# Kernel tuning notes

Measured on AMD Instinct MI355X. Metric: run time of the kernel, lower is better.

## Reference

```python
import jax, jax.numpy as jnp
import numpy as np

NUM_HEADS = 16
THETA = 10000.0


def _rotate_half(x):
    # interleaved pairs: (..., d) -> pairs (x1, x2) -> (-x2, x1) interleaved back
    x = x.reshape(x.shape[:-1] + (-1, 2))
    x1, x2 = x[..., 0], x[..., 1]
    return jnp.stack((-x2, x1), axis=-1).reshape(x.shape[:-2] + (-1,))


def _rope(x):
    # x: [B, H, S, d_k]
    d_k = x.shape[-1]
    seq_len = x.shape[-2]
    inv_freq = 1.0 / (THETA ** (jnp.arange(0, d_k, 2, dtype=jnp.float32) / d_k))  # [d_k/2]
    pos = jnp.arange(seq_len, dtype=jnp.float32)  # [S]
    theta = pos[:, None] * inv_freq[None, :]  # [S, d_k/2]
    cos = jnp.repeat(jnp.cos(theta), 2, axis=-1)  # [S, d_k]
    sin = jnp.repeat(jnp.sin(theta), 2, axis=-1)
    return x * cos + _rotate_half(x) * sin


def setup_inputs() -> dict:
    key = jax.random.key(0)
    kx, kq, kk, kv, ko = jax.random.split(key, 5)
    B, S, D = 2, 2048, 1024
    std = 1.0 / (2.0 * (2 * D) ** 0.5)
    return {
        "x": jax.random.normal(kx, (B, S, D), dtype=jnp.float32),
        "Wq": jax.random.normal(kq, (D, D), dtype=jnp.float32) * std,
        "Wk": jax.random.normal(kk, (D, D), dtype=jnp.float32) * std,
        "Wv": jax.random.normal(kv, (D, D), dtype=jnp.float32) * std,
        "Wo": jax.random.normal(ko, (D, D), dtype=jnp.float32) * std,
    }


def reference(x, Wq, Wk, Wv, Wo):
    B, S, D = x.shape
    H = NUM_HEADS
    d_k = D // H

    def split_heads(t):  # [B,S,D] -> [B,H,S,d_k]
        return t.reshape(B, S, H, d_k).transpose(0, 2, 1, 3)

    Q = split_heads(x @ Wq)
    K = split_heads(x @ Wk)
    V = split_heads(x @ Wv)

    Q = _rope(Q)
    K = _rope(K)

    scores = jnp.einsum("bhqd,bhkd->bhqk", Q, K) / jnp.sqrt(jnp.float32(d_k))
    causal = jnp.tril(jnp.ones((S, S), dtype=bool))  # [S,S]
    scores = jnp.where(causal[None, None], scores, -jnp.inf)
    attn = jax.nn.softmax(scores, axis=-1)
    out = jnp.einsum("bhqk,bhkd->bhqd", attn, V)  # [B,H,S,d_k]
    out = out.transpose(0, 2, 1, 3).reshape(B, S, D)
    return out @ Wo
```

## Files before the change

kernel.cpp:

```cpp
#include <hip/hip_runtime.h>
#include <cmath>


constexpr int Bz = 2, Sq = 2048, Dm = 1024, Hh = 16, DK = 64;
constexpr int Mrows = Bz * Sq;

typedef __attribute__((ext_vector_type(4))) float f32x4;
typedef __attribute__((ext_vector_type(2))) __bf16 bf16x2;
typedef __attribute__((ext_vector_type(4))) __bf16 bf16x4;
typedef __attribute__((ext_vector_type(8))) __bf16 bf16x8;
typedef __attribute__((ext_vector_type(8))) short short8v;

__device__ __forceinline__ f32x4 mfma16(bf16x8 a, bf16x8 b, f32x4 c) {
  return __builtin_amdgcn_mfma_f32_16x16x32_bf16(a, b, c, 0, 0, 0);
}
__device__ __forceinline__ short bfb(float x) {
  return __builtin_bit_cast(short, (__bf16)x);
}
__device__ __forceinline__ float fexp2(float x) {
#if __has_builtin(__builtin_amdgcn_exp2f)
  return __builtin_amdgcn_exp2f(x);
#else
  float r;
  asm("v_exp_f32 %0, %1" : "=v"(r) : "v"(x));
  return r;
#endif
}
__device__ __forceinline__ void gload16(const void* g, void* l) {
  __builtin_amdgcn_global_load_lds(
      (__attribute__((address_space(1))) void*)g,
      (__attribute__((address_space(3))) void*)l, 16, 0, 0);
}

__global__ __launch_bounds__(256) void prep_kernel(
    const float* __restrict__ x, const float* __restrict__ Wq,
    const float* __restrict__ Wk, const float* __restrict__ Wv,
    const float* __restrict__ Wo, __bf16* __restrict__ xb,
    __bf16* __restrict__ Wt, float2* __restrict__ tbl) {
  __shared__ float tile[32][33];
  const int bid = blockIdx.x, tid = threadIdx.x;
  if (bid < 2048) {
    int t = bid * 256 + tid;
    const float4* p = (const float4*)x + (size_t)t * 2;
    float4 a = p[0], b = p[1];
    bf16x8 o = {(__bf16)a.x, (__bf16)a.y, (__bf16)a.z, (__bf16)a.w,
                (__bf16)b.x, (__bf16)b.y, (__bf16)b.z, (__bf16)b.w};
    *(bf16x8*)(xb + (size_t)t * 8) = o;
  } else if (bid < 6144) {
    int wid = bid - 2048;
    int z = wid >> 10, rem = wid & 1023;
    const float* W = (z == 0) ? Wq : (z == 1) ? Wk : (z == 2) ? Wv : Wo;
    __bf16* out = Wt + (size_t)z * Dm * Dm;
    int r0 = (rem >> 5) * 32, c0 = (rem & 31) * 32;
    int r = tid >> 3, c4 = (tid & 7) * 4;
    float4 v = *(const float4*)&W[(size_t)(r0 + r) * Dm + c0 + c4];
    tile[r][c4] = v.x; tile[r][c4 + 1] = v.y;
    tile[r][c4 + 2] = v.z; tile[r][c4 + 3] = v.w;
    __syncthreads();
    int nl = tid >> 3, k4 = (tid & 7) * 4;
    bf16x4 o = {(__bf16)tile[k4][nl], (__bf16)tile[k4 + 1][nl],
                (__bf16)tile[k4 + 2][nl], (__bf16)tile[k4 + 3][nl]};
    *(bf16x4*)&out[(size_t)(c0 + nl) * Dm + r0 + k4] = o;
  } else {
    int t = (bid - 6144) * 256 + tid;
    int s = t >> 5, j = t & 31;
    float inv = exp2f(-13.287712379549449f * (1.0f / 32.0f) * (float)j);
    float sn, cs;
    sincosf((float)s * inv, &sn, &cs);
    tbl[t] = make_float2(cs, sn);
  }
}

__device__ __forceinline__ void gemm_core(const __bf16* __restrict__ A,
                                          const __bf16* __restrict__ Bt,
                                          char* smem, f32x4 (&acc)[4][4],
                                          int m0, int n0, int tid) {
  short* As = (short*)smem;
  short* Bs = (short*)(smem + 16384);
  const int lane = tid & 63, w = tid >> 6;
  const int qi = lane & 15, c = lane >> 4;
  const int wr = w >> 1, wc = w & 1;
  const int srow = lane >> 2, scol = (lane & 3) * 8;
  const __bf16* gA = A + (size_t)(m0 + w * 16 + srow) * Dm + scol;
  const __bf16* gB = Bt + (size_t)(n0 + w * 16 + srow) * Dm + scol;
  short* lA = As + w * 512;
  short* lB = Bs + w * 512;

  auto stage = [&](int cb, int k0) {
    gload16(gA + k0, lA + cb * 4096);
    gload16(gA + (size_t)64 * Dm + k0, lA + cb * 4096 + 2048);
    gload16(gB + k0, lB + cb * 4096);
    gload16(gB + (size_t)64 * Dm + k0, lB + cb * 4096 + 2048);
  };

#pragma unroll
  for (int i = 0; i < 4; ++i)
#pragma unroll
    for (int j = 0; j < 4; ++j) acc[i][j] = (f32x4){0.f, 0.f, 0.f, 0.f};

  stage(0, 0);
  __syncthreads();
  int cur = 0;
  for (int k0 = 0; k0 < Dm; k0 += 32) {
    if (k0 + 32 < Dm) stage(cur ^ 1, k0 + 32);
    bf16x8 af[4], bfv[4];
#pragma unroll
    for (int i = 0; i < 4; ++i) {
      af[i]  = *(bf16x8*)(As + cur * 4096 + (wr * 64 + i * 16 + qi) * 32 + c * 8);
      bfv[i] = *(bf16x8*)(Bs + cur * 4096 + (wc * 64 + i * 16 + qi) * 32 + c * 8);
    }
#pragma unroll
    for (int i = 0; i < 4; ++i)
#pragma unroll
      for (int j = 0; j < 4; ++j) acc[i][j] = mfma16(af[i], bfv[j], acc[i][j]);
    __syncthreads();
    cur ^= 1;
  }
}

__global__ __launch_bounds__(256) void gemm_qkv(
    const __bf16* __restrict__ xb, const __bf16* __restrict__ Wt,
    const float2* __restrict__ tbl, __bf16* __restrict__ Qb,
    __bf16* __restrict__ Kb, __bf16* __restrict__ Vt) {
  __shared__ __align__(16) char smem[34816];
  const int tid = threadIdx.x;
  const int bid = blockIdx.x;
  const int xcd = bid & 7, r8 = bid >> 3;
  const int mb = (xcd << 2) | (r8 & 3);
  const int zn = r8 >> 2;
  const int z = zn >> 3, nb = zn & 7;
  const int m0 = mb * 128, n0 = nb * 128;

  f32x4 acc[4][4];
  gemm_core(xb, Wt + (size_t)z * Dm * Dm, smem, acc, m0, n0, tid);

  const int lane = tid & 63, w = tid >> 6;
  const int qi = lane & 15, c = lane >> 4;
  const int wr = w >> 1, wc = w & 1;

  if (z == 2) {
    __syncthreads();
    short* T = (short*)smem;
#pragma unroll
    for (int i = 0; i < 4; ++i)
#pragma unroll
      for (int j = 0; j < 4; ++j) {
        int nl = wc * 64 + j * 16 + qi;
        int mbr = wr * 64 + i * 16 + c * 4;
        bf16x4 pk = {(__bf16)acc[i][j][0], (__bf16)acc[i][j][1],
                     (__bf16)acc[i][j][2], (__bf16)acc[i][j][3]};
        *(bf16x4*)(T + nl * 136 + mbr) = pk;
      }
    __syncthreads();
    short* C = (short*)Vt;
    int b = m0 >> 11, sb = m0 & (Sq - 1);
#pragma unroll
    for (int it = 0; it < 8; ++it) {
      int f = tid + it * 256;
      int nl = f >> 4, mc = f & 15;
      short8v v = *(short8v*)(T + nl * 136 + mc * 8);
      int ng = n0 + nl;
      int d = ng & (DK - 1), h = (ng >> 6) & (Hh - 1);
      *(short8v*)(C + ((size_t)(b * Hh + h) * DK + d) * Sq + sb + mc * 8) = v;
    }
  } else {
    __syncthreads();
    short* T = (short*)smem;
#pragma unroll
    for (int i = 0; i < 4; ++i)
#pragma unroll
      for (int j = 0; j < 4; ++j) {
        int nl = wc * 64 + j * 16 + qi;
        int mbr = wr * 64 + i * 16 + c * 4;
#pragma unroll
        for (int rr = 0; rr < 4; ++rr)
          T[(mbr + rr) * 136 + nl] = bfb(acc[i][j][rr]);
      }
    __syncthreads();
    const float sc = (z == 0) ? 0.18033688011112042f : 1.0f;
    short* C = (short*)((z == 0) ? Qb : Kb);
    const int b = m0 >> 11;
#pragma unroll
    for (int it = 0; it < 8; ++it) {
      int f = tid + it * 256;
      int ml = f >> 4, c16 = f & 15;
      bf16x8 v = *(bf16x8*)(T + ml * 136 + c16 * 8);
      int s = (m0 + ml) & (Sq - 1);
      int n = n0 + c16 * 8;
      int d0 = n & (DK - 1), h = (n >> 6) & (Hh - 1);
      int jj = d0 >> 1;
      float4 t01 = *(const float4*)&tbl[s * 32 + jj];
      float4 t23 = *(const float4*)&tbl[s * 32 + jj + 2];
      bf16x8 o;
      float x0 = (float)v[0], y0 = (float)v[1];
      o[0] = (__bf16)((x0 * t01.x - y0 * t01.y) * sc);
      o[1] = (__bf16)((y0 * t01.x + x0 * t01.y) * sc);
      float x1 = (float)v[2], y1 = (float)v[3];
      o[2] = (__bf16)((x1 * t01.z - y1 * t01.w) * sc);
      o[3] = (__bf16)((y1 * t01.z + x1 * t01.w) * sc);
      float x2 = (float)v[4], y2 = (float)v[5];
      o[4] = (__bf16)((x2 * t23.x - y2 * t23.y) * sc);
      o[5] = (__bf16)((y2 * t23.x + x2 * t23.y) * sc);
      float x3 = (float)v[6], y3 = (float)v[7];
      o[6] = (__bf16)((x3 * t23.z - y3 * t23.w) * sc);
      o[7] = (__bf16)((y3 * t23.z + x3 * t23.w) * sc);
      *(bf16x8*)(C + ((size_t)(b * Hh + h) * Sq + s) * DK + d0) = o;
    }
  }
}

__global__ __launch_bounds__(256) void gemm_o(
    const __bf16* __restrict__ AOb, const __bf16* __restrict__ Wto,
    float* __restrict__ C) {
  __shared__ __align__(16) char smem[34816];
  const int tid = threadIdx.x;
  const int bid = blockIdx.x;
  const int xcd = bid & 7, r8 = bid >> 3;
  const int mb = (xcd << 2) | (r8 & 3);
  const int nb = r8 >> 2;
  const int m0 = mb * 128, n0 = nb * 128;

  f32x4 acc[4][4];
  gemm_core(AOb, Wto, smem, acc, m0, n0, tid);

  const int lane = tid & 63, w = tid >> 6;
  const int qi = lane & 15, c = lane >> 4;
  const int wr = w >> 1, wc = w & 1;
  float* T32 = (float*)smem;

#pragma unroll
  for (int pass = 0; pass < 2; ++pass) {
    __syncthreads();
#pragma unroll
    for (int i2 = 0; i2 < 2; ++i2) {
      int i = pass * 2 + i2;
#pragma unroll
      for (int j = 0; j < 4; ++j) {
        int nl = wc * 64 + j * 16 + qi;
        int cm = wr * 32 + i2 * 16 + c * 4;
#pragma unroll
        for (int rr = 0; rr < 4; ++rr)
          T32[(cm + rr) * 132 + nl] = acc[i][j][rr];
      }
    }
    __syncthreads();
#pragma unroll
    for (int it = 0; it < 8; ++it) {
      int f = tid + it * 256;
      int cm = f >> 5, c4 = f & 31;
      float4 v = *(float4*)(T32 + cm * 132 + c4 * 4);
      int m = m0 + (cm >> 5) * 64 + pass * 32 + (cm & 31);
      *(float4*)&C[(size_t)m * Dm + n0 + c4 * 4] = v;
    }
  }
}

__global__ __launch_bounds__(512, 2) void attn_kernel(
    const __bf16* __restrict__ Qb, const __bf16* __restrict__ Kb,
    const __bf16* __restrict__ Vt, __bf16* __restrict__ AOb) {
  extern __shared__ __align__(16) char smem[];

  const int bid = blockIdx.x;
  const int xcd = bid & 7;
  const int idx = bid >> 3;
  const int bh = (xcd << 2) | (idx >> 3);
  const int j8 = idx & 7;
  const int b = bh >> 4, h = bh & (Hh - 1);
  const int tid = threadIdx.x, lane = tid & 63, w = tid >> 6;
  const int cg = w & 1, rg = (w >> 1) & 1, par = w >> 2;
  const int g = lane >> 4, qi = lane & 15;

  const __bf16* Qp = Qb + (size_t)bh * Sq * DK;
  const __bf16* Kp = Kb + (size_t)bh * Sq * DK;
  const __bf16* Vp = Vt + (size_t)bh * DK * Sq;

  char* myP = smem + 65536 + w * 4096;
  const int swz = (qi & 7) << 4;
  const int srow8 = lane >> 3, scol8 = lane & 7;
  const int srow4 = lane >> 4, scol16 = lane & 15;
  short* AOs = (short*)AOb;

  auto stage = [&](int cb, int t) {
    const int kbase = t * 128;
    char* Kd = smem + cb * 16384;
    char* Vd = smem + 32768 + cb * 16384;
#pragma unroll
    for (int s2 = 0; s2 < 2; ++s2) {
      int seg = w * 2 + s2;
      int r = seg * 8 + srow8;
      gload16(Kp + (size_t)(kbase + r) * DK + ((scol8 ^ (r & 7)) << 3),
              Kd + seg * 1024);
      int d = seg * 4 + srow4;
      int ss = (scol16 & 8) | ((scol16 ^ (d & 7)) & 7);
      gload16(Vp + (size_t)d * Sq + kbase + ss * 8, Vd + seg * 1024);
    }
  };

  auto tile = [&](int cb, bool domask, int kbase, int q0w,
                  const bf16x8 (&qf)[2][2], f32x4 (&acc)[2][4],
                  float (&m_)[2], float (&l_)[2]) {
    const char* Kt = smem + cb * 16384 + par * 8192;
    const char* Vv = smem + 32768 + cb * 16384;
    const int vpo = par * 128;

    bf16x8 kf[4][2];
#pragma unroll
    for (int bb = 0; bb < 4; ++bb) {
      int rr = 16 * bb + qi;
      kf[bb][0] = *(const bf16x8*)(Kt + rr * 128 + ((g ^ (rr & 7)) << 4));
      kf[bb][1] = *(const bf16x8*)(Kt + rr * 128 + (((g + 4) ^ (rr & 7)) << 4));
    }
    bf16x8 vf[4][2];
#pragma unroll
    for (int j = 0; j < 4; ++j) {
      int rr = 16 * j + qi;
      vf[j][0] = *(const bf16x8*)(Vv + rr * 256 + vpo + ((g ^ (rr & 7)) << 4));
      vf[j][1] =
          *(const bf16x8*)(Vv + rr * 256 + vpo + (((g + 4) ^ (rr & 7)) << 4));
    }

    f32x4 st[2][4];
    __builtin_amdgcn_s_setprio(1);
#pragma unroll
    for (int i = 0; i < 2; ++i)
#pragma unroll
      for (int bb = 0; bb < 4; ++bb) {
        st[i][bb] = mfma16(kf[bb][0], qf[i][0], (f32x4){0.f, 0.f, 0.f, 0.f});
        st[i][bb] = mfma16(kf[bb][1], qf[i][1], st[i][bb]);
      }
    __builtin_amdgcn_s_setprio(0);

    if (domask) {
#pragma unroll
      for (int i = 0; i < 2; ++i)
#pragma unroll
        for (int bb = 0; bb < 4; ++bb)
#pragma unroll
          for (int r = 0; r < 4; ++r)
            if (kbase + 16 * bb + 4 * g + r > q0w + i * 16 + qi)
              st[i][bb][r] = -1e30f;
    }

#pragma unroll
    for (int i = 0; i < 2; ++i) {
      float mb4[4];
#pragma unroll
      for (int bb = 0; bb < 4; ++bb)
        mb4[bb] = fmaxf(fmaxf(st[i][bb][0], st[i][bb][1]),
                        fmaxf(st[i][bb][2], st[i][bb][3]));
      float tpart = fmaxf(fmaxf(mb4[0], mb4[1]), fmaxf(mb4[2], mb4[3]));

      if (!__all(tpart <= m_[i] + 7.0f)) {
        float tmax = tpart;
        tmax = fmaxf(tmax, __shfl_xor(tmax, 16));
        tmax = fmaxf(tmax, __shfl_xor(tmax, 32));
        const float mnew = fmaxf(m_[i], tmax);
        const float corr = fexp2(m_[i] - mnew);
        l_[i] *= corr;
        float cr[4];
#pragma unroll
        for (int r = 0; r < 4; ++r) cr[r] = __shfl(corr, 4 * g + r);
#pragma unroll
        for (int j = 0; j < 4; ++j) {
          acc[i][j][0] *= cr[0]; acc[i][j][1] *= cr[1];
          acc[i][j][2] *= cr[2]; acc[i][j][3] *= cr[3];
        }
        m_[i] = mnew;
      }

      char* Pi = myP + i * 2048;
      float lsb[4];
#pragma unroll
      for (int bb = 0; bb < 4; ++bb) {
        float p0 = fexp2(st[i][bb][0] - m_[i]), p1 = fexp2(st[i][bb][1] - m_[i]);
        float p2 = fexp2(st[i][bb][2] - m_[i]), p3 = fexp2(st[i][bb][3] - m_[i]);
        lsb[bb] = (p0 + p1) + (p2 + p3);
        bf16x2 w0 = {(__bf16)p0, (__bf16)p1};
        bf16x2 w1 = {(__bf16)p2, (__bf16)p3};
        *(uint2*)(Pi + qi * 128 + ((32 * bb + 8 * g) ^ swz)) =
            make_uint2(__builtin_bit_cast(unsigned int, w0),
                       __builtin_bit_cast(unsigned int, w1));
      }
      l_[i] += (lsb[0] + lsb[1]) + (lsb[2] + lsb[3]);

      bf16x8 pa0 = *(bf16x8*)(Pi + qi * 128 + ((16 * g) ^ swz));
      bf16x8 pa1 = *(bf16x8*)(Pi + qi * 128 + ((64 + 16 * g) ^ swz));
      __builtin_amdgcn_s_setprio(1);
#pragma unroll
      for (int j = 0; j < 4; ++j) {
        acc[i][j] = mfma16(pa0, vf[j][0], acc[i][j]);
        acc[i][j] = mfma16(pa1, vf[j][1], acc[i][j]);
      }
      __builtin_amdgcn_s_setprio(0);
    }
  };

  auto run_mgroup = [&](int m) {
    const int q0w = 128 * m + cg * 64 + rg * 32;

    bf16x8 qf[2][2];
#pragma unroll
    for (int i = 0; i < 2; ++i) {
      qf[i][0] = *(const bf16x8*)(Qp + (q0w + i * 16 + qi) * DK + 8 * g);
      qf[i][1] = *(const bf16x8*)(Qp + (q0w + i * 16 + qi) * DK + 32 + 8 * g);
    }
    f32x4 acc[2][4];
#pragma unroll
    for (int i = 0; i < 2; ++i)
#pragma unroll
      for (int j = 0; j < 4; ++j) acc[i][j] = (f32x4){0.f, 0.f, 0.f, 0.f};
    float m_[2] = {-1e30f, -1e30f}, l_[2] = {0.f, 0.f};

    __syncthreads();
    stage(0, 0);

    int cur = 0;
    for (int t = 0; t < m; ++t) {
      __syncthreads();
      stage(cur ^ 1, t + 1);
      tile(cur, false, 0, q0w, qf, acc, m_, l_);
      cur ^= 1;
    }
    __syncthreads();
    if (!(par == 1 && cg == 0))
      tile(cur, par == cg, (2 * m + par) * 64, q0w, qf, acc, m_, l_);

    __syncthreads();
    char* Mb = smem + (cg * 2 + rg) * 9216 + lane * 144;
    if (par == 1) {
#pragma unroll
      for (int i = 0; i < 2; ++i)
#pragma unroll
        for (int j = 0; j < 4; ++j)
          *(f32x4*)(Mb + (i * 4 + j) * 16) = acc[i][j];
      *(float*)(Mb + 128) = m_[0];
      *(float*)(Mb + 132) = m_[1];
      *(float*)(Mb + 136) = l_[0];
      *(float*)(Mb + 140) = l_[1];
    }
    __syncthreads();
    if (par == 0) {
#pragma unroll
      for (int i = 0; i < 2; ++i) {
        float m1 = *(const float*)(Mb + 128 + i * 4);
        float l1 = *(const float*)(Mb + 136 + i * 4);
        const float mn = fmaxf(m_[i], m1);
        const float c0 = fexp2(m_[i] - mn), c1 = fexp2(m1 - mn);
        float lt = l_[i] * c0 + l1 * c1;
        lt += __shfl_xor(lt, 16);
        lt += __shfl_xor(lt, 32);
        float cr0[4], cr1[4], ir[4];
        const float inv = 1.f / lt;
#pragma unroll
        for (int r = 0; r < 4; ++r) {
          cr0[r] = __shfl(c0, 4 * g + r);
          cr1[r] = __shfl(c1, 4 * g + r);
          ir[r] = __shfl(inv, 4 * g + r);
        }
#pragma unroll
        for (int j = 0; j < 4; ++j) {
          f32x4 a1 = *(const f32x4*)(Mb + (i * 4 + j) * 16);
#pragma unroll
          for (int r = 0; r < 4; ++r) {
            float v = acc[i][j][r] * cr0[r] + a1[r] * cr1[r];
            AOs[((size_t)b * Sq + q0w + i * 16 + 4 * g + r) * Dm + h * DK +
                16 * j + qi] = bfb(v * ir[r]);
          }
        }
      }
    }
  };

  run_mgroup(15 - j8);
  run_mgroup(j8);
}

extern "C" void kernel_launch(void* const* d_in, const int* in_sizes, int n_in,
                              void* d_out, int out_size, void* d_ws,
                              size_t ws_size, hipStream_t stream) {
  const float* x  = (const float*)d_in[0];
  const float* Wq = (const float*)d_in[1];
  const float* Wk = (const float*)d_in[2];
  const float* Wv = (const float*)d_in[3];
  const float* Wo = (const float*)d_in[4];
  float* out = (float*)d_out;

  char* w = (char*)d_ws;
  __bf16* Qb  = (__bf16*)(w);
  __bf16* Kb  = (__bf16*)(w + (8u << 20));
  __bf16* Vt  = (__bf16*)(w + (16u << 20));
  __bf16* AOb = (__bf16*)(w + (24u << 20));
  __bf16* xb  = (__bf16*)(w + (32u << 20));
  __bf16* Wt  = (__bf16*)(w + (40u << 20));
  float2* tbl = (float2*)(w + (48u << 20));

  prep_kernel<<<6400, 256, 0, stream>>>(x, Wq, Wk, Wv, Wo, xb, Wt, tbl);
  gemm_qkv<<<768, 256, 0, stream>>>(xb, Wt, tbl, Qb, Kb, Vt);
  attn_kernel<<<256, 512, 98304, stream>>>(Qb, Kb, Vt, AOb);
  gemm_o<<<256, 256, 0, stream>>>(AOb, Wt + (size_t)3 * Dm * Dm, out);
}
```

Before: 97.33 us.

## Load GEMM fragments directly from global memory into registers, bypassing LDS

```diff
diff --git a/kernel.cpp b/kernel.cpp
--- a/kernel.cpp
+++ b/kernel.cpp
@@ -73,49 +73,52 @@
 
 __device__ __forceinline__ void gemm_core(const __bf16* __restrict__ A,
                                           const __bf16* __restrict__ Bt,
-                                          char* smem, f32x4 (&acc)[4][4],
+                                          f32x4 (&acc)[4][4],
                                           int m0, int n0, int tid) {
-  short* As = (short*)smem;
-  short* Bs = (short*)(smem + 16384);
   const int lane = tid & 63, w = tid >> 6;
   const int qi = lane & 15, c = lane >> 4;
   const int wr = w >> 1, wc = w & 1;
-  const int srow = lane >> 2, scol = (lane & 3) * 8;
-  const __bf16* gA = A + (size_t)(m0 + w * 16 + srow) * Dm + scol;
-  const __bf16* gB = Bt + (size_t)(n0 + w * 16 + srow) * Dm + scol;
-  short* lA = As + w * 512;
-  short* lB = Bs + w * 512;
-
-  auto stage = [&](int cb, int k0) {
-    gload16(gA + k0, lA + cb * 4096);
-    gload16(gA + (size_t)64 * Dm + k0, lA + cb * 4096 + 2048);
-    gload16(gB + k0, lB + cb * 4096);
-    gload16(gB + (size_t)64 * Dm + k0, lB + cb * 4096 + 2048);
-  };
+
+  const __bf16* pa[4];
+  const __bf16* pb[4];
+#pragma unroll
+  for (int i = 0; i < 4; ++i) {
+    pa[i] = A + (size_t)(m0 + wr * 64 + i * 16 + qi) * Dm + c * 8;
+    pb[i] = Bt + (size_t)(n0 + wc * 64 + i * 16 + qi) * Dm + c * 8;
+  }
 
 #pragma unroll
   for (int i = 0; i < 4; ++i)
 #pragma unroll
     for (int j = 0; j < 4; ++j) acc[i][j] = (f32x4){0.f, 0.f, 0.f, 0.f};
 
-  stage(0, 0);
-  __syncthreads();
-  int cur = 0;
-  for (int k0 = 0; k0 < Dm; k0 += 32) {
-    if (k0 + 32 < Dm) stage(cur ^ 1, k0 + 32);
-    bf16x8 af[4], bfv[4];
+  bf16x8 aC[4], bC[4], aN[4], bN[4];
+#pragma unroll
+  for (int i = 0; i < 4; ++i) {
+    aC[i] = *(const bf16x8*)(pa[i]);
+    bC[i] = *(const bf16x8*)(pb[i]);
+  }
+#pragma unroll
+  for (int t = 0; t < 31; ++t) {
 #pragma unroll
     for (int i = 0; i < 4; ++i) {
-      af[i]  = *(bf16x8*)(As + cur * 4096 + (wr * 64 + i * 16 + qi) * 32 + c * 8);
-      bfv[i] = *(bf16x8*)(Bs + cur * 4096 + (wc * 64 + i * 16 + qi) * 32 + c * 8);
+      aN[i] = *(const bf16x8*)(pa[i] + (t + 1) * 32);
+      bN[i] = *(const bf16x8*)(pb[i] + (t + 1) * 32);
     }
 #pragma unroll
     for (int i = 0; i < 4; ++i)
 #pragma unroll
-      for (int j = 0; j < 4; ++j) acc[i][j] = mfma16(af[i], bfv[j], acc[i][j]);
-    __syncthreads();
-    cur ^= 1;
+      for (int j = 0; j < 4; ++j) acc[i][j] = mfma16(aC[i], bC[j], acc[i][j]);
+#pragma unroll
+    for (int i = 0; i < 4; ++i) {
+      aC[i] = aN[i];
+      bC[i] = bN[i];
+    }
   }
+#pragma unroll
+  for (int i = 0; i < 4; ++i)
+#pragma unroll
+    for (int j = 0; j < 4; ++j) acc[i][j] = mfma16(aC[i], bC[j], acc[i][j]);
 }
 
 __global__ __launch_bounds__(256) void gemm_qkv(
@@ -132,7 +135,7 @@
   const int m0 = mb * 128, n0 = nb * 128;
 
   f32x4 acc[4][4];
-  gemm_core(xb, Wt + (size_t)z * Dm * Dm, smem, acc, m0, n0, tid);
+  gemm_core(xb, Wt + (size_t)z * Dm * Dm, acc, m0, n0, tid);
 
   const int lane = tid & 63, w = tid >> 6;
   const int qi = lane & 15, c = lane >> 4;
@@ -212,7 +215,7 @@
 __global__ __launch_bounds__(256) void gemm_o(
     const __bf16* __restrict__ AOb, const __bf16* __restrict__ Wto,
     float* __restrict__ C) {
-  __shared__ __align__(16) char smem[34816];
+  __shared__ __align__(16) char smem[33792];
   const int tid = threadIdx.x;
   const int bid = blockIdx.x;
   const int xcd = bid & 7, r8 = bid >> 3;
@@ -221,7 +224,7 @@
   const int m0 = mb * 128, n0 = nb * 128;
 
   f32x4 acc[4][4];
-  gemm_core(AOb, Wto, smem, acc, m0, n0, tid);
+  gemm_core(AOb, Wto, acc, m0, n0, tid);
 
   const int lane = tid & 63, w = tid >> 6;
   const int qi = lane & 15, c = lane >> 4;
```

After: 170.2 us. +74.9%, slower.
